# Optimization experiments

Hardware: AMD Instinct MI355X
Metric: run time of the kernel (lower is better)

Reference implementation:

```python
import jax, jax.numpy as jnp
import numpy as np

NQUBIT = 24
CHI = 512
Q = 2
MID_SCALE = 1.0 / 32.0  # 1/sqrt(Q*CHI): keeps the sequential bond-matrix product O(1)


def _to_c(x):
    # x[..., 0] = real part, x[..., 1] = imag part -> complex64
    return jax.lax.complex(x[..., 0], x[..., 1])


def setup_inputs() -> dict:
    key = jax.random.key(0)
    k1, k2, k3 = jax.random.split(key, 3)
    t_first = jax.random.normal(k1, (1, Q, CHI, 2), dtype=jnp.float32)
    t_mid = jax.random.normal(k2, (NQUBIT - 2, CHI, Q, CHI, 2), dtype=jnp.float32) * MID_SCALE
    t_last = jax.random.normal(k3, (CHI, Q, 1, 2), dtype=jnp.float32)
    return {"t_first": t_first, "t_mid": t_mid, "t_last": t_last}


def _sweep(t_first, t_mid, t_last):
    # Faithful translation of center_orthogonalization(c=-1):
    # left-to-right orthogonalize_left2right over sites 0..nqubit-2, dc=-1 (no
    # truncation), normalize=False. Each step: SVD of (Dl*q, Dr) reshape,
    # keep u as the new site tensor, absorb r = diag(s) @ vh into the next site
    # via einsum 'ab,bcd->acd'. Returns the center (last) tensor.
    tensors = [_to_c(t_first)] + [_to_c(t_mid[i]) for i in range(NQUBIT - 2)] + [_to_c(t_last)]
    for i in range(NQUBIT - 1):  # loop over sites (structural, shapes differ per site)
        t = tensors[i]
        Dl, q, Dr = t.shape
        u, s, vh = jnp.linalg.svd(t.reshape(Dl * q, Dr), full_matrices=False)
        tensors[i] = u.reshape(Dl, q, -1)            # left-orthogonal site tensor
        r = s.astype(vh.dtype)[:, None] * vh          # diag(s) @ vh, shape (k, Dr)
        tensors[i + 1] = jnp.einsum('ab,bcd->acd', r, tensors[i + 1])
    c = tensors[-1]  # center tensor, shape (CHI, Q, 1) complex64
    return jnp.stack([jnp.real(c), jnp.imag(c)], axis=-1)  # (CHI, Q, 1, 2) float32


def reference(t_first, t_mid, t_last):
    return _sweep(t_first, t_mid, t_last)
```

## Files before the change

kernel.cpp:

```cpp
#include <hip/hip_runtime.h>
#include <math.h>


#define LDV 513
typedef float2 cplx;

__device__ __forceinline__ cplx cmul(cplx a, cplx b){ return make_float2(a.x*b.x - a.y*b.y, a.x*b.y + a.y*b.x); }
__device__ __forceinline__ cplx cmulc(cplx a, cplx b){  return make_float2(a.x*b.x + a.y*b.y, a.x*b.y - a.y*b.x); }
__device__ __forceinline__ cplx cadd(cplx a, cplx b){ return make_float2(a.x+b.x, a.y+b.y); }
__device__ __forceinline__ cplx csub(cplx a, cplx b){ return make_float2(a.x-b.x, a.y-b.y); }
__device__ __forceinline__ cplx conjc(cplx a){ return make_float2(a.x, -a.y); }

#define EPS_S 5.9604645e-8f
#define UNFL_S 1.17549435e-38f
#define UW 512
#define UBLK 128

__device__ cplx g_A[1024*512];
__device__ cplx g_B[512*512];
__device__ cplx g_VTc[512*512];
__device__ cplx g_R[512*512];
__device__ cplx g_tauf[520];
__device__ cplx g_taup[520];
__device__ float g_d[520], g_e[520];
__device__ float g_VTr[LDV*LDV];
__device__ float g_VT2[LDV*LDV];
__device__ float g_W[LDV*LDV];
__device__ float g_z[520], g_zz[520], g_zorig[520], g_dtmp[520], g_ztmp[520], g_dsig[520];
__device__ double g_root[520];
__device__ int g_idxq[520], g_idx[520], g_idxp[520], g_rowmap[520];
__device__ int g_inode[80], g_ndiml[80], g_ndimr[80];
__device__ float g_sig[520];
__device__ int g_K, g_nlvl_, g_nd_;
__device__ float g_tol_, g_z1_;
__device__ double g_rho_;
__device__ float g_scq[520];
__device__ float g_betaq[520];
__device__ float g_rn[520];
__device__ float g_partC[UW];
__device__ float g_partR[UW];

__device__ __forceinline__ float wred(float v){
  for (int off=32;off;off>>=1) v+=__shfl_down(v,off);
  return v;
}
__device__ __forceinline__ float reduce512(const float* arr){
  __shared__ float sr[256];
  sr[threadIdx.x]=arr[threadIdx.x]+arr[threadIdx.x+256];
  __syncthreads();
  for (int s=128;s>0;s>>=1){
    if (threadIdx.x<s) sr[threadIdx.x]+=sr[threadIdx.x+s];
    __syncthreads();
  }
  float v=sr[0];
  __syncthreads();
  return v;
}

struct RfgOut { float beta; cplx tau; cplx scal; int skip; };
__device__ RfgOut clarfg_head(cplx alpha, float xn2){
  RfgOut o;
  if (xn2==0.f && alpha.y==0.f){
    o.beta=alpha.x; o.tau=make_float2(0.f,0.f); o.scal=make_float2(0.f,0.f); o.skip=1;
  } else {
    float anorm=sqrtf(alpha.x*alpha.x+alpha.y*alpha.y+xn2);
    float beta=(alpha.x>=0.f)?-anorm:anorm;
    o.beta=beta;
    o.tau=make_float2((beta-alpha.x)/beta,-alpha.y/beta);
    cplx dd=make_float2(alpha.x-beta,alpha.y);
    float dn=dd.x*dd.x+dd.y*dd.y;
    o.scal=make_float2(dd.x/dn,-dd.y/dn);
    o.skip=0;
  }
  return o;
}

__device__ float slapy2(float x, float y){
  float xa=fabsf(x), ya=fabsf(y);
  float w=fmaxf(xa,ya), z=fminf(xa,ya);
  if (z==0.f) return w;
  float q=z/w; return w*sqrtf(1.f+q*q);
}

__device__ void slartg(float f, float g, float* cs, float* sn, float* r){
  if (g==0.f){ *cs=1.f; *sn=0.f; *r=f; }
  else if (f==0.f){ *cs=0.f; *sn=(g>0.f)?1.f:-1.f; *r=fabsf(g); }
  else {
    float f1=fabsf(f);
    float d=sqrtf(f*f+g*g);
    *cs = f1/d;
    *r = (f>0.f)? d : -d;
    *sn = g / *r;
  }
}

__device__ void slas2(float f, float g, float h, float* ssmin, float* ssmax){
  float fa=fabsf(f), ga=fabsf(g), ha=fabsf(h);
  float fhmn=fminf(fa,ha), fhmx=fmaxf(fa,ha);
  if (fhmn==0.f){
    *ssmin=0.f;
    if (fhmx==0.f) *ssmax=ga;
    else { float mx=fmaxf(fhmx,ga), mn=fminf(fhmx,ga); float q=mn/mx; *ssmax=mx*sqrtf(1.f+q*q); }
  } else {
    if (ga < fhmx){
      float as=1.f+fhmn/fhmx, at=(fhmx-fhmn)/fhmx;
      float au=ga/fhmx; au=au*au;
      float c=2.f/(sqrtf(as*as+au)+sqrtf(at*at+au));
      *ssmin=fhmn*c; *ssmax=fhmx/c;
    } else {
      float au=fhmx/ga;
      if (au==0.f){ *ssmin=(fhmn*fhmx)/ga; *ssmax=ga; }
      else {
        float as=1.f+fhmn/fhmx, at=(fhmx-fhmn)/fhmx;
        float c=1.f/(sqrtf(1.f+(as*au)*(as*au))+sqrtf(1.f+(at*au)*(at*au)));
        *ssmin=(fhmn*c)*au; *ssmin=*ssmin+*ssmin;
        *ssmax=ga/(c+c);
      }
    }
  }
}

__device__ void slasv2(float f, float g, float h, float* ssmin, float* ssmax,
                       float* snr, float* csr, float* snl, float* csl){
  float ft=f, fa=fabsf(f), ht=h, ha=fabsf(h);
  int pmax=1;
  bool swap_=(ha>fa);
  if (swap_){ pmax=3; float t=ft; ft=ht; ht=t; t=fa; fa=ha; ha=t; }
  float gt=g, ga=fabsf(g);
  float clt=0.f, crt=0.f, slt=0.f, srt=0.f;
  if (ga==0.f){ *ssmin=ha; *ssmax=fa; clt=1.f; crt=1.f; slt=0.f; srt=0.f; }
  else {
    bool gasmal=true;
    if (ga>fa){
      pmax=2;
      if ((fa/ga) < EPS_S){
        gasmal=false;
        *ssmax=ga;
        if (ha>1.f) *ssmin=fa/(ga/ha); else *ssmin=(fa/ga)*ha;
        clt=1.f; slt=ht/gt; srt=1.f; crt=ft/gt;
      }
    }
    if (gasmal){
      float d=fa-ha;
      float l=(d==fa)?1.f:(d/fa);
      float mm=gt/ft;
      float t=2.f-l;
      float mm2=mm*mm, tt=t*t;
      float s=sqrtf(tt+mm2);
      float r=(l==0.f)?fabsf(mm):sqrtf(l*l+mm2);
      float a=0.5f*(s+r);
      *ssmin=ha/a; *ssmax=fa*a;
      if (mm2==0.f){
        if (l==0.f) t=copysignf(2.f,ft)*copysignf(1.f,gt);
        else t=gt/copysignf(d,ft)+mm/t;
      } else {
        t=(mm/(s+t)+mm/(r+l))*(1.f+a);
      }
      float l2=sqrtf(t*t+4.f);
      crt=2.f/l2; srt=t/l2;
      clt=(crt+srt*mm)/a;
      slt=(ht/ft)*srt/a;
    }
  }
  if (swap_){ *csl=srt; *snl=crt; *csr=slt; *snr=clt; }
  else      { *csl=clt; *snl=slt; *csr=crt; *snr=srt; }
  float tsign=0.f;
  if (pmax==1) tsign=copysignf(1.f,*csr)*copysignf(1.f,*csl)*copysignf(1.f,f);
  if (pmax==2) tsign=copysignf(1.f,*snr)*copysignf(1.f,*csl)*copysignf(1.f,g);
  if (pmax==3) tsign=copysignf(1.f,*snr)*copysignf(1.f,*snl)*copysignf(1.f,h);
  *ssmax=copysignf(*ssmax,tsign);
  *ssmin=copysignf(*ssmin,tsign*copysignf(1.f,f)*copysignf(1.f,h));
}

__device__ void slasr_f(int mrows, int ncols, const float* c1, const float* s1, float* a, int lda){
  for (int j=1;j<=mrows-1;++j){
    float ct=c1[j], st=s1[j];
    if (ct!=1.f || st!=0.f){
      float* rj=&a[(j-1)*lda]; float* rj1=&a[j*lda];
      for (int i=0;i<ncols;++i){
        float tmp=rj1[i];
        rj1[i]=ct*tmp-st*rj[i];
        rj[i]=st*tmp+ct*rj[i];
      }
    }
  }
}
__device__ void slasr_b(int mrows, int ncols, const float* c1, const float* s1, float* a, int lda){
  for (int j=mrows-1;j>=1;--j){
    float ct=c1[j], st=s1[j];
    if (ct!=1.f || st!=0.f){
      float* rj=&a[(j-1)*lda]; float* rj1=&a[j*lda];
      for (int i=0;i<ncols;++i){
        float tmp=rj1[i];
        rj1[i]=ct*tmp-st*rj[i];
        rj[i]=st*tmp+ct*rj[i];
      }
    }
  }
}

__device__ void sbdsqr_u(int n, int ncvt, float* d, float* e, float* vt, int ldvt){
  const int MAXITR=6;
  if (n==0) return;
  if (n>1){
    int nm1=n-1, nm12=nm1+nm1, nm13=nm12+nm1;
    float wk[112];
    float tolmul=10.f;
    float tol=tolmul*EPS_S;
    float smax=0.f;
    for (int i=1;i<=n;i++) smax=fmaxf(smax,fabsf(d[i]));
    for (int i=1;i<=n-1;i++) smax=fmaxf(smax,fabsf(e[i]));
    float sminl=0.f, thresh;
    {
      float sminoa=fabsf(d[1]);
      if (sminoa!=0.f){
        float mu=sminoa;
        for (int i=2;i<=n;i++){
          mu=fabsf(d[i])*(mu/(mu+fabsf(e[i-1])));
          sminoa=fminf(sminoa,mu);
          if (sminoa==0.f) break;
        }
      }
      sminoa=sminoa/sqrtf((float)n);
      thresh=fmaxf(tol*sminoa,(float)(MAXITR*n*n)*UNFL_S);
    }
    int M=n, iter=0, maxit=MAXITR*n*n;
    int oldll=-1, oldm=-1, idir=0;
    while (1){
      if (M<=1) break;
      if (iter>maxit) break;
      int ll=0; bool split=false;
      smax=fabsf(d[M]);
      for (int lll=1;lll<=M-1;++lll){
        ll=M-lll;
        float abss=fabsf(d[ll]), abse=fabsf(e[ll]);
        if (abse<=thresh){ split=true; break; }
        smax=fmaxf(smax,fmaxf(abss,abse));
      }
      if (!split) ll=0;
      else {
        e[ll]=0.f;
        if (ll==M-1){ M=M-1; continue; }
      }
      ll=ll+1;
      if (ll==M-1){
        float sigmn,sigmx,sinr,cosr,sinl,cosl;
        slasv2(d[M-1],e[M-1],d[M],&sigmn,&sigmx,&sinr,&cosr,&sinl,&cosl);
        d[M-1]=sigmx; e[M-1]=0.f; d[M]=sigmn;
        if (ncvt>0){
          float* x=&vt[(M-2)*ldvt]; float* y=&vt[(M-1)*ldvt];
          for (int c=0;c<ncvt;c++){ float xv=x[c],yv=y[c]; x[c]=cosr*xv+sinr*yv; y[c]=cosr*yv-sinr*xv; }
        }
        M-=2; continue;
      }
      if (ll>oldm || M<oldll) idir=(fabsf(d[ll])>=fabsf(d[M]))?1:2;
      bool conv=false;
      if (idir==1){
        if (fabsf(e[M-1])<=fabsf(tol)*fabsf(d[M])){ e[M-1]=0.f; conv=true; }
        else {
          float mu=fabsf(d[ll]); sminl=mu;
          for (int lll=ll;lll<=M-1;++lll){
            if (fabsf(e[lll])<=tol*mu){ e[lll]=0.f; conv=true; break; }
            mu=fabsf(d[lll+1])*(mu/(mu+fabsf(e[lll])));
            sminl=fminf(sminl,mu);
          }
        }
      } else {
        if (fabsf(e[ll])<=fabsf(tol)*fabsf(d[ll])){ e[ll]=0.f; conv=true; }
        else {
          float mu=fabsf(d[M]); sminl=mu;
          for (int lll=M-1;lll>=ll;--lll){
            if (fabsf(e[lll])<=tol*mu){ e[lll]=0.f; conv=true; break; }
            mu=fabsf(d[lll])*(mu/(mu+fabsf(e[lll])));
            sminl=fminf(sminl,mu);
          }
        }
      }
      if (conv) continue;
      oldll=ll; oldm=M;
      float shift=0.f, rr;
      if ((float)n*tol*(sminl/smax)<=fmaxf(EPS_S,0.01f*tol)) shift=0.f;
      else {
        float sll;
        if (idir==1){ sll=fabsf(d[ll]); slas2(d[M-1],e[M-1],d[M],&shift,&rr); }
        else        { sll=fabsf(d[M]);  slas2(d[ll],e[ll],d[ll+1],&shift,&rr); }
        if (sll>0.f){ float q=shift/sll; if (q*q<EPS_S) shift=0.f; }
      }
      iter += M-ll;
      if (shift==0.f){
        if (idir==1){
          float cs=1.f, oldcs=1.f, sn=0.f, oldsn=0.f;
          for (int i=ll;i<=M-1;++i){
            float c2,r1;
            slartg(d[i]*cs,e[i],&c2,&sn,&r1); cs=c2;
            if (i>ll) e[i-1]=oldsn*r1;
            float oc2;
            slartg(oldcs*r1,d[i+1]*sn,&oc2,&oldsn,&d[i]); oldcs=oc2;
            wk[i-ll+1]=cs; wk[i-ll+1+nm1]=sn;
          }
          float h=d[M]*cs; d[M]=h*oldcs; e[M-1]=h*oldsn;
          if (ncvt>0) slasr_f(M-ll+1,ncvt,wk,wk+nm1,&vt[(ll-1)*ldvt],ldvt);
          if (fabsf(e[M-1])<=thresh) e[M-1]=0.f;
        } else {
          float cs=1.f, oldcs=1.f, sn=0.f, oldsn=0.f;
          for (int i=M;i>=ll+1;--i){
            float c2,r1;
            slartg(d[i]*cs,e[i-1],&c2,&sn,&r1); cs=c2;
            if (i<M) e[i]=oldsn*r1;
            float oc2;
            slartg(oldcs*r1,d[i-1]*sn,&oc2,&oldsn,&d[i]); oldcs=oc2;
            wk[i-ll]=cs; wk[i-ll+nm1]=-sn;
            wk[i-ll+nm12]=oldcs; wk[i-ll+nm13]=-oldsn;
          }
          float h=d[ll]*cs; d[ll]=h*oldcs; e[ll]=h*oldsn;
          if (ncvt>0) slasr_b(M-ll+1,ncvt,wk+nm12,wk+nm13,&vt[(ll-1)*ldvt],ldvt);
          if (fabsf(e[ll])<=thresh) e[ll]=0.f;
        }
      } else {
        if (idir==1){
          float f=(fabsf(d[ll])-shift)*(copysignf(1.f,d[ll])+shift/d[ll]);
          float g=e[ll], cosr,sinr,cosl,sinl,r1;
          for (int i=ll;i<=M-1;++i){
            slartg(f,g,&cosr,&sinr,&r1);
            if (i>ll) e[i-1]=r1;
            f=cosr*d[i]+sinr*e[i];
            e[i]=cosr*e[i]-sinr*d[i];
            g=sinr*d[i+1];
            d[i+1]=cosr*d[i+1];
            slartg(f,g,&cosl,&sinl,&r1);
            d[i]=r1;
            f=cosl*e[i]+sinl*d[i+1];
            d[i+1]=cosl*d[i+1]-sinl*e[i];
            if (i<M-1){ g=sinl*e[i+1]; e[i+1]=cosl*e[i+1]; }
            wk[i-ll+1]=cosr; wk[i-ll+1+nm1]=sinr;
            wk[i-ll+1+nm12]=cosl; wk[i-ll+1+nm13]=sinl;
          }
          e[M-1]=f;
          if (ncvt>0) slasr_f(M-ll+1,ncvt,wk,wk+nm1,&vt[(ll-1)*ldvt],ldvt);
          if (fabsf(e[M-1])<=thresh) e[M-1]=0.f;
        } else {
          float f=(fabsf(d[M])-shift)*(copysignf(1.f,d[M])+shift/d[M]);
          float g=e[M-1], cosr,sinr,cosl,sinl,r1;
          for (int i=M;i>=ll+1;--i){
            slartg(f,g,&cosr,&sinr,&r1);
            if (i<M) e[i]=r1;
            f=cosr*d[i]+sinr*e[i-1];
            e[i-1]=cosr*e[i-1]-sinr*d[i];
            g=sinr*d[i-1];
            d[i-1]=cosr*d[i-1];
            slartg(f,g,&cosl,&sinl,&r1);
            d[i]=r1;
            f=cosl*e[i-1]+sinl*d[i-1];
            d[i-1]=cosl*d[i-1]-sinl*e[i-1];
            if (i>ll+1){ g=sinl*e[i-2]; e[i-2]=cosl*e[i-2]; }
            wk[i-ll]=cosr; wk[i-ll+nm1]=-sinr;
            wk[i-ll+nm12]=cosl; wk[i-ll+nm13]=-sinl;
          }
          e[ll]=f;
          if (fabsf(e[ll])<=thresh) e[ll]=0.f;
          if (ncvt>0) slasr_b(M-ll+1,ncvt,wk+nm12,wk+nm13,&vt[(ll-1)*ldvt],ldvt);
        }
      }
    }
  }
  for (int i=1;i<=n;i++){
    if (d[i]<0.f){
      d[i]=-d[i];
      if (ncvt>0){ float* row=&vt[(i-1)*ldvt]; for (int c=0;c<ncvt;c++) row[c]=-row[c]; }
    }
  }
  for (int i=1;i<=n-1;i++){
    int isub=1; float smin2=d[1];
    for (int j=2;j<=n+1-i;j++){ if (d[j]<=smin2){ isub=j; smin2=d[j]; } }
    if (isub!=n+1-i){
      d[isub]=d[n+1-i]; d[n+1-i]=smin2;
      if (ncvt>0){
        float* a=&vt[(isub-1)*ldvt]; float* b=&vt[(n-i)*ldvt];
        for (int c=0;c<ncvt;c++){ float t=a[c]; a[c]=b[c]; b[c]=t; }
      }
    }
  }
}

__device__ void slasdq_u(int sqre, int n, int ncvt, float* d, float* e, float* vt, int ldvt){
  if (n==0) return;
  float cwk[33], swk[33];
  int np1=n+1;
  if (sqre==1){
    for (int i=1;i<=n-1;i++){
      float cs,sn,r; slartg(d[i],e[i],&cs,&sn,&r);
      d[i]=r; e[i]=sn*d[i+1]; d[i+1]=cs*d[i+1];
      cwk[i]=cs; swk[i]=sn;
    }
    { float cs,sn,r; slartg(d[n],e[n],&cs,&sn,&r);
      d[n]=r; e[n]=0.f; cwk[n]=cs; swk[n]=sn; }
    if (ncvt>0) slasr_f(np1,ncvt,cwk,swk,vt,ldvt);
    for (int i=1;i<=n-1;i++){
      float cs,sn,r; slartg(d[i],e[i],&cs,&sn,&r);
      d[i]=r; e[i]=sn*d[i+1]; d[i+1]=cs*d[i+1];
    }
  }
  sbdsqr_u(n,ncvt,d,e,vt,ldvt);
  for (int i=1;i<=n;i++){
    int isub=i; float smin2=d[i];
    for (int j=i+1;j<=n;j++){ if (d[j]<smin2){ isub=j; smin2=d[j]; } }
    if (isub!=i){
      d[isub]=d[i]; d[i]=smin2;
      if (ncvt>0){
        float* a=&vt[(isub-1)*ldvt]; float* b=&vt[(i-1)*ldvt];
        for (int c=0;c<ncvt;c++){ float t=a[c]; a[c]=b[c]; b[c]=t; }
      }
    }
  }
}

__device__ void slamrg(int n1, int n2, const float* a, int s1, int s2, int* idx){
  int n1sv=n1, n2sv=n2, i=1;
  int ind1=(s1>0)?1:n1;
  int ind2=(s2>0)?(1+n1):(n1+n2);
  while (n1sv>0 && n2sv>0){
    if (a[ind1]<=a[ind2]){ idx[i++]=ind1; ind1+=s1; n1sv--; }
    else { idx[i++]=ind2; ind2+=s2; n2sv--; }
  }
  if (n1sv==0){ for(;n2sv>0;n2sv--){ idx[i++]=ind2; ind2+=s2; } }
  else { for(;n1sv>0;n1sv--){ idx[i++]=ind1; ind1+=s1; } }
}

__device__ void slasdt(int n, int* lvl, int* nd, int* inode, int* ndiml, int* ndimr, int msub){
  int maxn=(n>1)?n:1;
  float temp=logf((float)maxn/(float)(msub+1))/logf(2.f);
  *lvl=(int)temp+1;
  int i=n/2;
  inode[1]=i+1; ndiml[1]=i; ndimr[1]=n-i-1;
  int il=0, ir=1, llst=1;
  for (int nl=1;nl<=*lvl-1;++nl){
    for (int j=0;j<=llst-1;++j){
      il+=2; ir+=2;
      int nc=llst+j;
      ndiml[il]=ndiml[nc]/2;
      ndimr[il]=ndiml[nc]-ndiml[il]-1;
      inode[il]=inode[nc]-ndimr[il]-1;
      ndiml[ir]=ndimr[nc]/2;
      ndimr[ir]=ndimr[nc]-ndiml[ir]-1;
      inode[ir]=inode[nc]+ndiml[ir]+1;
    }
    llst*=2;
  }
  *nd=llst*2-1;
}

__device__ void merge_node(int nl, int nr, int sqre, float* d, int* idxq,
                           float alpha, float beta, float* VT, int ld)
{
  const int tid=threadIdx.x, nth=blockDim.x;
  const int n=nl+nr+1, m=n+sqre, nlp1=nl+1, nlp2=nl+2;
  if (tid==0){
    float* z=g_z;
    float z1=alpha*VT[(nlp1-1)*ld+(nlp1-1)];
    z[1]=z1; g_z1_=z1;
    for (int i=nl;i>=1;--i){
      z[i+1]=alpha*VT[(i-1)*ld+(nlp1-1)];
      d[i+1]=d[i];
      idxq[i+1]=idxq[i]+1;
    }
    for (int i=nlp2;i<=m;++i) z[i]=beta*VT[(i-1)*ld+(nlp2-1)];
    d[1]=0.f;
    for (int i=nlp2;i<=n;++i) idxq[i]+=nlp1;
    for (int i=2;i<=n;++i){ g_dtmp[i]=d[idxq[i]]; g_ztmp[i]=z[idxq[i]]; }
    slamrg(nl,nr,g_dtmp+1,1,1,g_idx+1);
    for (int i=2;i<=n;++i){
      int idxi=1+g_idx[i];
      d[i]=g_dtmp[idxi];
      z[i]=g_ztmp[idxi];
    }
    float tol=fmaxf(fabsf(alpha),fabsf(beta));
    tol=8.f*EPS_S*fmaxf(fabsf(d[n]),tol);
    g_tol_=tol;
    int K=1, K2=n+1, jprev=0, j;
    for (j=2;j<=n;++j){
      if (fabsf(z[j])<=tol){
        K2--; g_idxp[K2]=j;
        if (j==n){ jprev=0; break; }
      } else { jprev=j; break; }
    }
    if (jprev>0){
      j=jprev;
      for (;;){
        j++;
        if (j>n) break;
        if (fabsf(z[j])<=tol){ K2--; g_idxp[K2]=j; }
        else {
          if (fabsf(d[j]-d[jprev])<=tol){
            float s_=z[jprev], c_=z[j];
            float tau_=slapy2(c_,s_);
            c_/=tau_; s_=-s_/tau_;
            z[j]=tau_; z[jprev]=0.f;
            int idxjp=idxq[g_idx[jprev]+1];
            int idxj =idxq[g_idx[j]+1];
            if (idxjp<=nlp1) idxjp--;
            if (idxj <=nlp1) idxj--;
            float* xr=&VT[(idxjp-1)*ld];
            float* yr=&VT[(idxj-1)*ld];
            for (int cc=0;cc<m;++cc){
              float xv=xr[cc], yv=yr[cc];
              xr[cc]=c_*xv+s_*yv;
              yr[cc]=c_*yv-s_*xv;
            }
            K2--; g_idxp[K2]=jprev;
            jprev=j;
          } else {
            K++; g_zz[K]=z[jprev]; g_idxp[K]=jprev;
            jprev=j;
          }
        }
      }
      K++; g_zz[K]=z[jprev]; g_idxp[K]=jprev;
    }
    g_K=K;
    for (int jj=2;jj<=n;++jj){
      g_dsig[jj]=d[g_idxp[jj]];
      int rm=idxq[g_idx[g_idxp[jj]]+1];
      if (rm<=nlp1) rm--;
      g_rowmap[jj]=rm;
    }
  }
  __syncthreads();
  int K=g_K;
  for (int t=tid;t<(n-1)*m;t+=nth){
    int jj=2+t/m, cc=t%m;
    g_VT2[(jj-1)*LDV+cc]=VT[(g_rowmap[jj]-1)*ld+cc];
  }
  __syncthreads();
  if (tid==0){
    float tol=g_tol_;
    g_dsig[1]=0.f;
    float hlftol=tol*0.5f;
    if (fabsf(g_dsig[2])<=hlftol) g_dsig[2]=hlftol;
    float z1=g_z1_;
    float c_=1.f, s_=0.f;
    if (m>n){
      float t1=slapy2(z1,g_z[m]);
      if (t1<=tol){ c_=1.f; s_=0.f; g_z[1]=tol; }
      else { g_z[1]=t1; c_=z1/t1; s_=g_z[m]/t1; }
    } else {
      if (fabsf(z1)<=tol) g_z[1]=tol; else g_z[1]=z1;
    }
    for (int jj=2;jj<=K;++jj) g_z[jj]=g_zz[jj];
    if (m>n){
      for (int i=1;i<=nlp1;++i){
        float v=VT[(nlp1-1)*ld+(i-1)];
        VT[(m-1)*ld+(i-1)]=-s_*v;
        g_VT2[(i-1)]=c_*v;
      }
      for (int i=nlp2;i<=m;++i){
        float v=VT[(m-1)*ld+(i-1)];
        g_VT2[(i-1)]=s_*v;
        VT[(m-1)*ld+(i-1)]=c_*v;
      }
    } else {
      for (int i=1;i<=m;++i) g_VT2[(i-1)]=VT[(nlp1-1)*ld+(i-1)];
    }
    for (int jj=K+1;jj<=n;++jj) d[jj]=g_dsig[jj];
    double rho=0.0;
    for (int jj=1;jj<=K;++jj){ double zz2=(double)g_z[jj]; rho+=zz2*zz2; g_zorig[jj]=g_z[jj]; }
    g_rho_=rho;
  }
  __syncthreads();
  for (int t=tid;t<(n-K)*m;t+=nth){
    int jj=K+1+t/m, cc=t%m;
    VT[(jj-1)*ld+cc]=g_VT2[(jj-1)*LDV+cc];
  }
  __syncthreads();
  if (K==1){
    if (tid==0){
      d[1]=fabsf(g_z[1]);
      for (int cc=0;cc<m;++cc) VT[cc]=g_VT2[cc];
      slamrg(1,n-1,d,1,-1,idxq);
    }
    __syncthreads();
    return;
  }
  {
    double rho=g_rho_;
    for (int i=1+tid;i<=K;i+=nth){
      double di=(double)g_dsig[i];
      double lo=di*di, hi;
      if (i<K){ double dn=(double)g_dsig[i+1]; hi=dn*dn; }
      else { double dn=(double)g_dsig[K]; hi=dn*dn+rho; }
      for (int it=0;it<110;++it){
        double mid=0.5*(lo+hi);
        double f=1.0;
        for (int j=1;j<=K;++j){
          double dj=(double)g_dsig[j];
          double zj=(double)g_z[j];
          f+=zj*zj/(dj*dj-mid);
        }
        if (f>=0.0) hi=mid; else lo=mid;
      }
      g_root[i]=0.5*(lo+hi);
      d[i]=(float)sqrt(g_root[i]);
    }
  }
  __syncthreads();
  for (int i=1+tid;i<=K;i+=nth){
    double di=(double)g_dsig[i], di2=di*di;
    double p=di2-g_root[K];
    for (int j=1;j<=i-1;++j){
      double dj=(double)g_dsig[j];
      p*=(di2-g_root[j])/((di-dj)*(di+dj));
    }
    for (int j=i;j<=K-1;++j){
      double dj1=(double)g_dsig[j+1];
      p*=(di2-g_root[j])/((di-dj1)*(di+dj1));
    }
    g_ztmp[i]=copysignf((float)sqrt(fabs(p)),g_zorig[i]);
  }
  __syncthreads();
  for (int i=1+tid;i<=K;i+=nth) g_z[i]=g_ztmp[i];
  __syncthreads();
  for (int i=1+tid;i<=K;i+=nth){
    double xi=g_root[i];
    double nrm=0.0;
    for (int j=1;j<=K;++j){
      double dj=(double)g_dsig[j];
      double w=(double)g_z[j]/(dj*dj-xi);
      g_W[(i-1)*LDV+(j-1)]=(float)w;
      nrm+=w*w;
    }
    float inv=(float)(1.0/sqrt(nrm));
    for (int j=1;j<=K;++j) g_W[(i-1)*LDV+(j-1)]*=inv;
  }
  __syncthreads();
  for (int t=tid;t<K*m;t+=nth){
    int i=1+t/m, cc=t%m;
    float acc=0.f;
    for (int j=1;j<=K;++j)
      acc=fmaf(g_W[(i-1)*LDV+(j-1)],g_VT2[(j-1)*LDV+cc],acc);
    VT[(i-1)*ld+cc]=acc;
  }
  __syncthreads();
  if (tid==0) slamrg(K,n-K,d,1,-1,idxq);
  __syncthreads();
}

__global__ __launch_bounds__(1024) void k_sbdsdc(int n){
  const int tid=threadIdx.x, lane=tid&63, wv=tid>>6;
  for (int t=tid;t<n*n;t+=1024)
    g_VTr[(t/n)*LDV+(t%n)]=((t/n)==(t%n))?1.f:0.f;
  __syncthreads();
  if (n<=25){
    if (tid==0){
      slasdq_u(0,n,n,g_d,g_e,g_VTr,LDV);
      for (int j=1;j<=n;++j) g_idxq[j]=j;
    }
    __syncthreads();
  } else {
    if (tid==0){
      int lvl,nd;
      slasdt(n,&lvl,&nd,g_inode,g_ndiml,g_ndimr,25);
      g_nlvl_=lvl; g_nd_=nd;
    }
    __syncthreads();
    int nd=g_nd_, nlvl=g_nlvl_;
    int ndb1=(nd+1)/2;
    int ntask=(nd-ndb1+1)*2;
    for (int task=wv;task<ntask;task+=16){
      if (lane==0){
        int node=ndb1+(task>>1);
        int ic=g_inode[node], nl=g_ndiml[node], nr=g_ndimr[node];
        if ((task&1)==0){
          int nlf=ic-nl;
          slasdq_u(1,nl,nl+1,g_d+(nlf-1),g_e+(nlf-1),&g_VTr[(nlf-1)*LDV+(nlf-1)],LDV);
          for (int j2=1;j2<=nl;++j2) g_idxq[nlf-1+j2]=j2;
        } else {
          int nrf=ic+1;
          int sq=(node==nd)?0:1;
          slasdq_u(sq,nr,nr+sq,g_d+(nrf-1),g_e+(nrf-1),&g_VTr[(nrf-1)*LDV+(nrf-1)],LDV);
          for (int j2=1;j2<=nr;++j2) g_idxq[nrf-1+j2]=j2;
        }
      }
    }
    __syncthreads();
    for (int lvl=nlvl;lvl>=1;--lvl){
      int lf=(lvl==1)?1:(1<<(lvl-1));
      int llast=(lvl==1)?1:(2*lf-1);
      for (int node=lf;node<=llast;++node){
        int ic=g_inode[node], nl=g_ndiml[node], nr=g_ndimr[node];
        int nlf=ic-nl;
        int sq=(node==llast)?0:1;
        float alpha=g_d[ic], beta=g_e[ic];
        merge_node(nl,nr,sq,g_d+(nlf-1),g_idxq+(nlf-1),alpha,beta,
                   &g_VTr[(nlf-1)*LDV+(nlf-1)],LDV);
      }
    }
  }
  __syncthreads();
  for (int t=tid;t<n*512;t+=1024){
    int i=t/512, c=t%512;
    int o=g_idxq[n-i];
    float v=(c<n)?g_VTr[(o-1)*LDV+c]:0.f;
    g_VTc[i*512+c]=make_float2(v,0.f);
    if (c==0) g_sig[i]=g_d[o];
  }
}

__global__ void k_m0(const float* __restrict__ tf){
  int i=blockIdx.x*blockDim.x+threadIdx.x;
  if (i<1024) g_A[i]=make_float2(tf[2*i],tf[2*i+1]);
}

__global__ __launch_bounds__(1024) void k_lq(int m){
  const int n=512;
  const int tid=threadIdx.x, lane=tid&63, wv=tid>>6;
  __shared__ float s_part[16];
  __shared__ cplx s_tau, s_scal;
  __shared__ float s_beta; __shared__ int s_skip;
  for (int i=1;i<=m;++i){
    for (int c=i+tid;c<=n;c+=1024) g_A[(i-1)*512+(c-1)].y=-g_A[(i-1)*512+(c-1)].y;
    __syncthreads();
    float sq=0.f;
    for (int c=i+1+tid;c<=n;c+=1024){
      cplx a=g_A[(i-1)*512+(c-1)];
      sq=fmaf(a.x,a.x,fmaf(a.y,a.y,sq));
    }
    sq=wred(sq);
    if (lane==0) s_part[wv]=sq;
    __syncthreads();
    if (tid==0){
      float xn2=0.f; for (int w=0;w<16;w++) xn2+=s_part[w];
      RfgOut o=clarfg_head(g_A[(i-1)*512+(i-1)],xn2);
      s_beta=o.beta; s_tau=o.tau; s_scal=o.scal; s_skip=o.skip;
      g_tauf[i]=o.tau;
    }
    __syncthreads();
    if (!s_skip){
      for (int c=i+1+tid;c<=n;c+=1024)
        g_A[(i-1)*512+(c-1)]=cmul(g_A[(i-1)*512+(c-1)],s_scal);
    }
    __syncthreads();
    if (!s_skip){
      cplx tau=s_tau;
      for (int r=i+1+wv;r<=m;r+=16){
        cplx acc=make_float2(0.f,0.f);
        for (int c=i+lane;c<=n;c+=64){
          cplx u=(c==i)?make_float2(1.f,0.f):g_A[(i-1)*512+(c-1)];
          acc=cadd(acc,cmul(g_A[(r-1)*512+(c-1)],u));
        }
        acc.x=wred(acc.x); acc.y=wred(acc.y);
        acc.x=__shfl(acc.x,0); acc.y=__shfl(acc.y,0);
        cplx tw=cmul(tau,acc);
        for (int c=i+lane;c<=n;c+=64){
          cplx u=(c==i)?make_float2(1.f,0.f):g_A[(i-1)*512+(c-1)];
          g_A[(r-1)*512+(c-1)]=csub(g_A[(r-1)*512+(c-1)],cmul(tw,conjc(u)));
        }
      }
    }
    __syncthreads();
    if (tid==0) g_A[(i-1)*512+(i-1)]=make_float2(s_beta,0.f);
    __syncthreads();
  }
}

__global__ void k_copyL(int m){
  int t=blockIdx.x*blockDim.x+threadIdx.x;
  if (t>=m*m) return;
  int r=t/m, c=t%m;
  g_B[r*512+c]=(c<=r)?g_A[r*512+c]:make_float2(0.f,0.f);
}
__global__ void k_copyM(){
  int t=blockIdx.x*blockDim.x+threadIdx.x;
  if (t<512*512) g_B[t]=g_A[t];
}
__global__ void k_copyR_b(){
  int t=blockIdx.x*blockDim.x+threadIdx.x;
  if (t>=512*512) return;
  int r=t/512, c=t%512;
  g_B[t]=(c>r)?g_A[t]:((c==r)?make_float2(g_betaq[r+1],0.f):make_float2(0.f,0.f));
}

__global__ __launch_bounds__(1024) void k_bd(int n){
  const int tid=threadIdx.x, lane=tid&63, wv=tid>>6;
  __shared__ float s_part[16];
  __shared__ cplx s_tau, s_scal;
  __shared__ float s_beta; __shared__ int s_skip;
  for (int i=1;i<=n;++i){
    float sq=0.f;
    for (int r=i+1+tid;r<=n;r+=1024){
      cplx a=g_B[(r-1)*512+(i-1)];
      sq=fmaf(a.x,a.x,fmaf(a.y,a.y,sq));
    }
    sq=wred(sq);
    if (lane==0) s_part[wv]=sq;
    __syncthreads();
    if (tid==0){
      float xn2=0.f; for (int w=0;w<16;w++) xn2+=s_part[w];
      RfgOut o=clarfg_head(g_B[(i-1)*512+(i-1)],xn2);
      s_beta=o.beta; s_tau=o.tau; s_scal=o.scal; s_skip=o.skip;
      g_d[i]=o.beta;
    }
    __syncthreads();
    if (!s_skip){
      for (int r=i+1+tid;r<=n;r+=1024)
        g_B[(r-1)*512+(i-1)]=cmul(g_B[(r-1)*512+(i-1)],s_scal);
    }
    __syncthreads();
    if (!s_skip){
      cplx tauc=conjc(s_tau);
      for (int c=i+1+wv;c<=n;c+=16){
        cplx acc=make_float2(0.f,0.f);
        for (int r=i+lane;r<=n;r+=64){
          cplx v=(r==i)?make_float2(1.f,0.f):g_B[(r-1)*512+(i-1)];
          acc=cadd(acc,cmulc(v,g_B[(r-1)*512+(c-1)]));
        }
        acc.x=wred(acc.x); acc.y=wred(acc.y);
        acc.x=__shfl(acc.x,0); acc.y=__shfl(acc.y,0);
        cplx tw=cmul(tauc,acc);
        for (int r=i+lane;r<=n;r+=64){
          cplx v=(r==i)?make_float2(1.f,0.f):g_B[(r-1)*512+(i-1)];
          g_B[(r-1)*512+(c-1)]=csub(g_B[(r-1)*512+(c-1)],cmul(tw,v));
        }
      }
    }
    __syncthreads();
    if (tid==0) g_B[(i-1)*512+(i-1)]=make_float2(s_beta,0.f);
    __syncthreads();
    if (i<n){
      for (int c=i+1+tid;c<=n;c+=1024) g_B[(i-1)*512+(c-1)].y=-g_B[(i-1)*512+(c-1)].y;
      __syncthreads();
      float sq2=0.f;
      for (int c=i+2+tid;c<=n;c+=1024){
        cplx a=g_B[(i-1)*512+(c-1)];
        sq2=fmaf(a.x,a.x,fmaf(a.y,a.y,sq2));
      }
      sq2=wred(sq2);
      if (lane==0) s_part[wv]=sq2;
      __syncthreads();
      if (tid==0){
        float xn2=0.f; for (int w=0;w<16;w++) xn2+=s_part[w];
        RfgOut o=clarfg_head(g_B[(i-1)*512+(i)],xn2);
        s_beta=o.beta; s_tau=o.tau; s_scal=o.scal; s_skip=o.skip;
        g_e[i]=o.beta; g_taup[i]=o.tau;
      }
      __syncthreads();
      if (!s_skip){
        for (int c=i+2+tid;c<=n;c+=1024)
          g_B[(i-1)*512+(c-1)]=cmul(g_B[(i-1)*512+(c-1)],s_scal);
      }
      __syncthreads();
      if (!s_skip){
        cplx tau=s_tau;
        for (int r=i+1+wv;r<=n;r+=16){
          cplx acc=make_float2(0.f,0.f);
          for (int c=i+1+lane;c<=n;c+=64){
            cplx v=(c==i+1)?make_float2(1.f,0.f):g_B[(i-1)*512+(c-1)];
            acc=cadd(acc,cmul(g_B[(r-1)*512+(c-1)],v));
          }
          acc.x=wred(acc.x); acc.y=wred(acc.y);
          acc.x=__shfl(acc.x,0); acc.y=__shfl(acc.y,0);
          cplx tw=cmul(tau,acc);
          for (int c=i+1+lane;c<=n;c+=64){
            cplx v=(c==i+1)?make_float2(1.f,0.f):g_B[(i-1)*512+(c-1)];
            g_B[(r-1)*512+(c-1)]=csub(g_B[(r-1)*512+(c-1)],cmul(tw,conjc(v)));
          }
        }
      }
      __syncthreads();
      for (int c=i+2+tid;c<=n;c+=1024) g_B[(i-1)*512+(c-1)].y=-g_B[(i-1)*512+(c-1)].y;
      if (tid==0) g_B[(i-1)*512+(i)]=make_float2(s_beta,0.f);
      __syncthreads();
    }
  }
}

__global__ __launch_bounds__(1024) void k_applyPH(int n){
  const int tid=threadIdx.x, lane=tid&63, wv=tid>>6;
  for (int i=n-1;i>=1;--i){
    cplx tau=g_taup[i];
    if (tau.x==0.f && tau.y==0.f) continue;
    cplx tauc=conjc(tau);
    for (int r=1+wv;r<=n;r+=16){
      cplx acc=make_float2(0.f,0.f);
      for (int c=i+1+lane;c<=n;c+=64){
        cplx v=(c==i+1)?make_float2(1.f,0.f):conjc(g_B[(i-1)*512+(c-1)]);
        acc=cadd(acc,cmul(g_VTc[(r-1)*512+(c-1)],v));
      }
      acc.x=wred(acc.x); acc.y=wred(acc.y);
      acc.x=__shfl(acc.x,0); acc.y=__shfl(acc.y,0);
      cplx tw=cmul(tauc,acc);
      for (int c=i+1+lane;c<=n;c+=64){
        cplx vb=(c==i+1)?make_float2(1.f,0.f):g_B[(i-1)*512+(c-1)];
        g_VTc[(r-1)*512+(c-1)]=csub(g_VTc[(r-1)*512+(c-1)],cmul(tw,vb));
      }
    }
    __syncthreads();
  }
}

__global__ __launch_bounds__(1024) void k_applyQlq(int m){
  const int tid=threadIdx.x, lane=tid&63, wv=tid>>6;
  for (int i=m;i>=1;--i){
    cplx tau=g_tauf[i];
    if (tau.x==0.f && tau.y==0.f) continue;
    cplx tauc=conjc(tau);
    for (int r=1+wv;r<=m;r+=16){
      cplx acc=make_float2(0.f,0.f);
      for (int c=i+lane;c<=512;c+=64){
        cplx u=(c==i)?make_float2(1.f,0.f):g_A[(i-1)*512+(c-1)];
        acc=cadd(acc,cmul(g_VTc[(r-1)*512+(c-1)],u));
      }
      acc.x=wred(acc.x); acc.y=wred(acc.y);
      acc.x=__shfl(acc.x,0); acc.y=__shfl(acc.y,0);
      cplx tw=cmul(tauc,acc);
      for (int c=i+lane;c<=512;c+=64){
        cplx u=(c==i)?make_float2(1.f,0.f):g_A[(i-1)*512+(c-1)];
        g_VTc[(r-1)*512+(c-1)]=csub(g_VTc[(r-1)*512+(c-1)],cmul(tw,conjc(u)));
      }
    }
    __syncthreads();
  }
}


__global__ __launch_bounds__(256) void u_qr_pro(){
  __shared__ float sr[256];
  int t=threadIdx.x;
  float sq=0.f;
  for (int r=2+t;r<=1024;r+=256){ cplx a=g_A[(r-1)*512]; sq=fmaf(a.x,a.x,fmaf(a.y,a.y,sq)); }
  sr[t]=sq; __syncthreads();
  for (int s=128;s>0;s>>=1){ if (t<s) sr[t]+=sr[t+s]; __syncthreads(); }
  if (t==0) g_scq[1]=sr[0];
}

__global__ __launch_bounds__(256) void u_qr(int j){
  const int m=1024, n=512;
  int gtid=blockIdx.x*256+threadIdx.x;
  int lane=gtid&63, gw=gtid>>6;
  float xn2=g_scq[j];
  cplx alpha=g_A[(j-1)*512+(j-1)];
  RfgOut o=clarfg_head(alpha,xn2);
  if (gtid==0) g_betaq[j]=o.beta;
  cplx tauc=conjc(o.tau);
  float nsq=0.f;
  for (int c=j+1+gw;c<=n;c+=UW){
    cplx acc=make_float2(0.f,0.f);
    for (int r=j+lane;r<=m;r+=64){
      cplx v=(r==j)?make_float2(1.f,0.f):cmul(g_A[(r-1)*512+(j-1)],o.scal);
      acc=cadd(acc,cmulc(v,g_A[(r-1)*512+(c-1)]));
    }
    acc.x=wred(acc.x); acc.y=wred(acc.y);
    acc.x=__shfl(acc.x,0); acc.y=__shfl(acc.y,0);
    cplx tw=cmul(tauc,acc);
    for (int r=j+lane;r<=m;r+=64){
      cplx v=(r==j)?make_float2(1.f,0.f):cmul(g_A[(r-1)*512+(j-1)],o.scal);
      cplx nv=csub(g_A[(r-1)*512+(c-1)],cmul(tw,v));
      g_A[(r-1)*512+(c-1)]=nv;
      if (c==j+1 && r>=j+2) nsq=fmaf(nv.x,nv.x,fmaf(nv.y,nv.y,nsq));
    }
  }
  if (gw==0){
    nsq=wred(nsq);
    if (lane==0) g_scq[j+1]=nsq;
  }
}

__global__ __launch_bounds__(512) void u_bd_pro(){
  int t=threadIdx.x;
  float sq=0.f;
  for (int r=2+t;r<=512;r+=512){ cplx a=g_B[(r-1)*512]; sq=fmaf(a.x,a.x,fmaf(a.y,a.y,sq)); }
  g_partR[t]=sq;
}

__global__ __launch_bounds__(256) void u_bd_col(int i){
  const int n=512;
  float xn2c=reduce512(g_partR);
  int gtid=blockIdx.x*256+threadIdx.x;
  int lane=gtid&63, gw=gtid>>6;
  cplx alpha=g_B[(i-1)*512+(i-1)];
  RfgOut oc=clarfg_head(alpha,xn2c);
  if (gtid==0) g_d[i]=oc.beta;
  cplx tauc=conjc(oc.tau);
  float nsqA=0.f;
  for (int c=i+1+gw;c<=n;c+=UW){
    cplx acc=make_float2(0.f,0.f);
    for (int r=i+lane;r<=n;r+=64){
      cplx v=(r==i)?make_float2(1.f,0.f):cmul(g_B[(r-1)*512+(i-1)],oc.scal);
      acc=cadd(acc,cmulc(v,g_B[(r-1)*512+(c-1)]));
    }
    acc.x=wred(acc.x); acc.y=wred(acc.y);
    acc.x=__shfl(acc.x,0); acc.y=__shfl(acc.y,0);
    cplx tw=cmul(tauc,acc);
    for (int r=i+lane;r<=n;r+=64){
      cplx v=(r==i)?make_float2(1.f,0.f):cmul(g_B[(r-1)*512+(i-1)],oc.scal);
      cplx nv=csub(g_B[(r-1)*512+(c-1)],cmul(tw,v));
      g_B[(r-1)*512+(c-1)]=nv;
      if (r==i && c>=i+2) nsqA=fmaf(nv.x,nv.x,fmaf(nv.y,nv.y,nsqA));
    }
  }
  if (lane==0) g_partC[gw]=nsqA;
}

__global__ __launch_bounds__(256) void u_bd_row(int i){
  const int n=512;
  float xn2r=reduce512(g_partC);
  int gtid=blockIdx.x*256+threadIdx.x;
  int lane=gtid&63, gw=gtid>>6;
  cplx alphar=conjc(g_B[(i-1)*512+(i)]);
  RfgOut orr=clarfg_head(alphar,xn2r);
  if (gtid==0){ g_e[i]=orr.beta; g_taup[i]=orr.tau; g_rn[i]=xn2r; }
  float nsqB=0.f;
  for (int r=i+1+gw;r<=n;r+=UW){
    cplx acc=make_float2(0.f,0.f);
    for (int c=i+1+lane;c<=n;c+=64){
      cplx v=(c==i+1)?make_float2(1.f,0.f):cmul(conjc(g_B[(i-1)*512+(c-1)]),orr.scal);
      acc=cadd(acc,cmul(g_B[(r-1)*512+(c-1)],v));
    }
    acc.x=wred(acc.x); acc.y=wred(acc.y);
    acc.x=__shfl(acc.x,0); acc.y=__shfl(acc.y,0);
    cplx tw=cmul(orr.tau,acc);
    for (int c=i+1+lane;c<=n;c+=64){
      cplx v=(c==i+1)?make_float2(1.f,0.f):cmul(conjc(g_B[(i-1)*512+(c-1)]),orr.scal);
      cplx nv=csub(g_B[(r-1)*512+(c-1)],cmul(tw,conjc(v)));
      g_B[(r-1)*512+(c-1)]=nv;
      if (c==i+1 && r>=i+2) nsqB=fmaf(nv.x,nv.x,fmaf(nv.y,nv.y,nsqB));
    }
  }
  if (lane==0) g_partR[gw]=nsqB;
}

__global__ __launch_bounds__(256) void u_ph(){
  const int n=512;
  int b=blockIdx.x;
  int wv=threadIdx.x>>6, lane=threadIdx.x&63;
  int r=b*4+wv+1;
  for (int i=n-1;i>=1;--i){
    cplx alphar=conjc(g_B[(i-1)*512+(i)]);
    RfgOut o=clarfg_head(alphar,g_rn[i]);
    if (o.skip) continue;
    cplx tauc=conjc(o.tau);
    cplx acc=make_float2(0.f,0.f);
    for (int c=i+1+lane;c<=n;c+=64){
      cplx v=(c==i+1)?make_float2(1.f,0.f):cmul(conjc(g_B[(i-1)*512+(c-1)]),o.scal);
      acc=cadd(acc,cmul(g_VTc[(r-1)*512+(c-1)],v));
    }
    acc.x=wred(acc.x); acc.y=wred(acc.y);
    acc.x=__shfl(acc.x,0); acc.y=__shfl(acc.y,0);
    cplx tw=cmul(tauc,acc);
    for (int c=i+1+lane;c<=n;c+=64){
      cplx v=(c==i+1)?make_float2(1.f,0.f):cmul(conjc(g_B[(i-1)*512+(c-1)]),o.scal);
      g_VTc[(r-1)*512+(c-1)]=csub(g_VTc[(r-1)*512+(c-1)],cmul(tw,conjc(v)));
    }
  }
}

__global__ void k_formR(int kk){
  int t=blockIdx.x*blockDim.x+threadIdx.x;
  if (t>=kk*512) return;
  float s=g_sig[t/512];
  cplx v=g_VTc[t];
  g_R[t]=make_float2(s*v.x,s*v.y);
}

__global__ void k_next(const float* __restrict__ tmid, int site){
  int row=blockIdx.x;
  int a=row>>1, s=row&1;
  int b=blockIdx.y*blockDim.x+threadIdx.x;
  const float* base=tmid+(size_t)site*512*2*512*2;
  cplx acc=make_float2(0.f,0.f);
  for (int c=0;c<512;++c){
    cplx r=g_R[a*512+c];
    size_t off=((((size_t)c)*2+s)*512+b)*2;
    cplx x=make_float2(base[off],base[off+1]);
    acc=cadd(acc,cmul(r,x));
  }
  g_A[row*512+b]=acc;
}

__global__ void k_final(const float* __restrict__ tlast, float* __restrict__ out){
  int a=blockIdx.x*blockDim.x+threadIdx.x;
  if (a>=512) return;
  for (int s=0;s<2;++s){
    cplx acc=make_float2(0.f,0.f);
    for (int c=0;c<512;++c){
      cplx r=g_R[a*512+c];
      cplx x=make_float2(tlast[(c*2+s)*2],tlast[(c*2+s)*2+1]);
      acc=cadd(acc,cmul(r,x));
    }
    out[a*4+s*2+0]=acc.x;
    out[a*4+s*2+1]=acc.y;
  }
}

extern "C" void kernel_launch(void* const* d_in, const int* in_sizes, int n_in,
                              void* d_out, int out_size, void* d_ws, size_t ws_size,
                              hipStream_t stream) {
  const float* t_first=(const float*)d_in[0];
  const float* t_mid  =(const float*)d_in[1];
  const float* t_last =(const float*)d_in[2];
  float* out=(float*)d_out;
  (void)in_sizes; (void)n_in; (void)d_ws; (void)ws_size; (void)out_size;

  k_m0<<<dim3(4),256,0,stream>>>(t_first);

  int rows=2;
  for (int site=0;site<23;++site){
    int mm=rows;
    int nb=(mm<512)?mm:512;
    if (mm<512){
      k_lq<<<1,1024,0,stream>>>(mm);
      k_copyL<<<dim3((mm*mm+255)/256),256,0,stream>>>(mm);
      k_bd<<<1,1024,0,stream>>>(mm);
      k_sbdsdc<<<1,1024,0,stream>>>(mm);
      k_applyPH<<<1,1024,0,stream>>>(mm);
      k_applyQlq<<<1,1024,0,stream>>>(mm);
    } else {
      if (mm==512){
        k_copyM<<<dim3((512*512+255)/256),256,0,stream>>>();
      } else {
        u_qr_pro<<<1,256,0,stream>>>();
        for (int j=1;j<=512;++j) u_qr<<<UBLK,256,0,stream>>>(j);
        k_copyR_b<<<dim3((512*512+255)/256),256,0,stream>>>();
      }
      u_bd_pro<<<1,512,0,stream>>>();
      for (int i=1;i<=512;++i){
        u_bd_col<<<UBLK,256,0,stream>>>(i);
        if (i<512) u_bd_row<<<UBLK,256,0,stream>>>(i);
      }
      k_sbdsdc<<<1,1024,0,stream>>>(512);
      u_ph<<<UBLK,256,0,stream>>>();
    }
    k_formR<<<dim3((nb*512+255)/256),256,0,stream>>>(nb);
    if (site<22){
      k_next<<<dim3(2*nb,2),256,0,stream>>>(t_mid,site);
      rows=2*nb;
    } else {
      k_final<<<dim3(2),256,0,stream>>>(t_last,out);
    }
  }
}
```

Before: 1.080 s.

## Replace per-step kernel launches with persistent kernels using a software grid barrier

The per-column Householder QR launches (512 kernels) and the bidiagonalization launches (about 1023 kernels) are each merged into one persistent kernel with 128 blocks, which synchronize through an atomic-counter grid barrier. This removes launch overhead and inter-kernel gaps on the roughly 1500 serialized small steps per large site. The barrier relies on all 128 blocks being co-resident without a cooperative launch. On timeout it sets a fail flag and silently stops synchronizing, which could corrupt results.

Result: slower. 1.567 s, median of 2 (+45.1%).

```diff
diff --git a/kernel.cpp b/kernel.cpp
--- a/kernel.cpp
+++ b/kernel.cpp
@@ -39,6 +39,32 @@
 __device__ float g_rn[520];
 __device__ float g_partC[UW];
 __device__ float g_partR[UW];
+__device__ unsigned g_barc = 0;
+__device__ unsigned g_barg = 0;
+__device__ int g_barfail = 0;
+
+__device__ __forceinline__ void gbar(){
+  __syncthreads();
+  if (threadIdx.x==0){
+    if (!g_barfail){
+      __threadfence();
+      unsigned gen=__hip_atomic_load(&g_barg,__ATOMIC_RELAXED,__HIP_MEMORY_SCOPE_AGENT);
+      unsigned prev=__hip_atomic_fetch_add(&g_barc,1u,__ATOMIC_ACQ_REL,__HIP_MEMORY_SCOPE_AGENT);
+      if (prev+1u==(unsigned)gridDim.x){
+        __hip_atomic_store(&g_barc,0u,__ATOMIC_RELAXED,__HIP_MEMORY_SCOPE_AGENT);
+        __hip_atomic_store(&g_barg,gen+1u,__ATOMIC_RELEASE,__HIP_MEMORY_SCOPE_AGENT);
+      } else {
+        long k=0;
+        while (__hip_atomic_load(&g_barg,__ATOMIC_ACQUIRE,__HIP_MEMORY_SCOPE_AGENT)==gen){
+          __builtin_amdgcn_s_sleep(2);
+          if (++k>(1L<<24)){ g_barfail=1; break; }
+        }
+      }
+      __threadfence();
+    }
+  }
+  __syncthreads();
+}
 
 __device__ __forceinline__ float wred(float v){
   for (int off=32;off;off>>=1) v+=__shfl_down(v,off);
@@ -921,110 +947,116 @@
 }
 
 
-__global__ __launch_bounds__(256) void u_qr_pro(){
-  __shared__ float sr[256];
-  int t=threadIdx.x;
-  float sq=0.f;
-  for (int r=2+t;r<=1024;r+=256){ cplx a=g_A[(r-1)*512]; sq=fmaf(a.x,a.x,fmaf(a.y,a.y,sq)); }
-  sr[t]=sq; __syncthreads();
-  for (int s=128;s>0;s>>=1){ if (t<s) sr[t]+=sr[t+s]; __syncthreads(); }
-  if (t==0) g_scq[1]=sr[0];
-}
-
-__global__ __launch_bounds__(256) void u_qr(int j){
+__global__ __launch_bounds__(256) void pk_qr(){
   const int m=1024, n=512;
-  int gtid=blockIdx.x*256+threadIdx.x;
-  int lane=gtid&63, gw=gtid>>6;
-  float xn2=g_scq[j];
-  cplx alpha=g_A[(j-1)*512+(j-1)];
-  RfgOut o=clarfg_head(alpha,xn2);
-  if (gtid==0) g_betaq[j]=o.beta;
-  cplx tauc=conjc(o.tau);
-  float nsq=0.f;
-  for (int c=j+1+gw;c<=n;c+=UW){
-    cplx acc=make_float2(0.f,0.f);
-    for (int r=j+lane;r<=m;r+=64){
-      cplx v=(r==j)?make_float2(1.f,0.f):cmul(g_A[(r-1)*512+(j-1)],o.scal);
-      acc=cadd(acc,cmulc(v,g_A[(r-1)*512+(c-1)]));
-    }
-    acc.x=wred(acc.x); acc.y=wred(acc.y);
-    acc.x=__shfl(acc.x,0); acc.y=__shfl(acc.y,0);
-    cplx tw=cmul(tauc,acc);
-    for (int r=j+lane;r<=m;r+=64){
-      cplx v=(r==j)?make_float2(1.f,0.f):cmul(g_A[(r-1)*512+(j-1)],o.scal);
-      cplx nv=csub(g_A[(r-1)*512+(c-1)],cmul(tw,v));
-      g_A[(r-1)*512+(c-1)]=nv;
-      if (c==j+1 && r>=j+2) nsq=fmaf(nv.x,nv.x,fmaf(nv.y,nv.y,nsq));
-    }
-  }
-  if (gw==0){
-    nsq=wred(nsq);
-    if (lane==0) g_scq[j+1]=nsq;
-  }
-}
-
-__global__ __launch_bounds__(512) void u_bd_pro(){
-  int t=threadIdx.x;
-  float sq=0.f;
-  for (int r=2+t;r<=512;r+=512){ cplx a=g_B[(r-1)*512]; sq=fmaf(a.x,a.x,fmaf(a.y,a.y,sq)); }
-  g_partR[t]=sq;
-}
-
-__global__ __launch_bounds__(256) void u_bd_col(int i){
+  const int gtid=blockIdx.x*256+threadIdx.x;
+  const int lane=gtid&63, gw=gtid>>6;
+  {
+    __shared__ float sr[256];
+    int t=threadIdx.x;
+    float sq=0.f;
+    for (int r=2+t;r<=1024;r+=256){ cplx a=g_A[(r-1)*512]; sq=fmaf(a.x,a.x,fmaf(a.y,a.y,sq)); }
+    sr[t]=sq; __syncthreads();
+    for (int s=128;s>0;s>>=1){ if (t<s) sr[t]+=sr[t+s]; __syncthreads(); }
+    if (gtid==0) g_scq[1]=sr[0];
+  }
+  gbar();
+  for (int j=1;j<=n;++j){
+    float xn2=g_scq[j];
+    cplx alpha=g_A[(j-1)*512+(j-1)];
+    RfgOut o=clarfg_head(alpha,xn2);
+    if (gtid==0) g_betaq[j]=o.beta;
+    cplx tauc=conjc(o.tau);
+    float nsq=0.f;
+    for (int c=j+1+gw;c<=n;c+=UW){
+      cplx acc=make_float2(0.f,0.f);
+      for (int r=j+lane;r<=m;r+=64){
+        cplx v=(r==j)?make_float2(1.f,0.f):cmul(g_A[(r-1)*512+(j-1)],o.scal);
+        acc=cadd(acc,cmulc(v,g_A[(r-1)*512+(c-1)]));
+      }
+      acc.x=wred(acc.x); acc.y=wred(acc.y);
+      acc.x=__shfl(acc.x,0); acc.y=__shfl(acc.y,0);
+      cplx tw=cmul(tauc,acc);
+      for (int r=j+lane;r<=m;r+=64){
+        cplx v=(r==j)?make_float2(1.f,0.f):cmul(g_A[(r-1)*512+(j-1)],o.scal);
+        cplx nv=csub(g_A[(r-1)*512+(c-1)],cmul(tw,v));
+        g_A[(r-1)*512+(c-1)]=nv;
+        if (c==j+1 && r>=j+2) nsq=fmaf(nv.x,nv.x,fmaf(nv.y,nv.y,nsq));
+      }
+    }
+    if (gw==0){
+      nsq=wred(nsq);
+      if (lane==0) g_scq[j+1]=nsq;
+    }
+    gbar();
+  }
+}
+
+__global__ __launch_bounds__(256) void pk_bd(){
   const int n=512;
-  float xn2c=reduce512(g_partR);
-  int gtid=blockIdx.x*256+threadIdx.x;
-  int lane=gtid&63, gw=gtid>>6;
-  cplx alpha=g_B[(i-1)*512+(i-1)];
-  RfgOut oc=clarfg_head(alpha,xn2c);
-  if (gtid==0) g_d[i]=oc.beta;
-  cplx tauc=conjc(oc.tau);
-  float nsqA=0.f;
-  for (int c=i+1+gw;c<=n;c+=UW){
-    cplx acc=make_float2(0.f,0.f);
-    for (int r=i+lane;r<=n;r+=64){
-      cplx v=(r==i)?make_float2(1.f,0.f):cmul(g_B[(r-1)*512+(i-1)],oc.scal);
-      acc=cadd(acc,cmulc(v,g_B[(r-1)*512+(c-1)]));
-    }
-    acc.x=wred(acc.x); acc.y=wred(acc.y);
-    acc.x=__shfl(acc.x,0); acc.y=__shfl(acc.y,0);
-    cplx tw=cmul(tauc,acc);
-    for (int r=i+lane;r<=n;r+=64){
-      cplx v=(r==i)?make_float2(1.f,0.f):cmul(g_B[(r-1)*512+(i-1)],oc.scal);
-      cplx nv=csub(g_B[(r-1)*512+(c-1)],cmul(tw,v));
-      g_B[(r-1)*512+(c-1)]=nv;
-      if (r==i && c>=i+2) nsqA=fmaf(nv.x,nv.x,fmaf(nv.y,nv.y,nsqA));
-    }
-  }
-  if (lane==0) g_partC[gw]=nsqA;
-}
-
-__global__ __launch_bounds__(256) void u_bd_row(int i){
-  const int n=512;
-  float xn2r=reduce512(g_partC);
-  int gtid=blockIdx.x*256+threadIdx.x;
-  int lane=gtid&63, gw=gtid>>6;
-  cplx alphar=conjc(g_B[(i-1)*512+(i)]);
-  RfgOut orr=clarfg_head(alphar,xn2r);
-  if (gtid==0){ g_e[i]=orr.beta; g_taup[i]=orr.tau; g_rn[i]=xn2r; }
-  float nsqB=0.f;
-  for (int r=i+1+gw;r<=n;r+=UW){
-    cplx acc=make_float2(0.f,0.f);
-    for (int c=i+1+lane;c<=n;c+=64){
-      cplx v=(c==i+1)?make_float2(1.f,0.f):cmul(conjc(g_B[(i-1)*512+(c-1)]),orr.scal);
-      acc=cadd(acc,cmul(g_B[(r-1)*512+(c-1)],v));
-    }
-    acc.x=wred(acc.x); acc.y=wred(acc.y);
-    acc.x=__shfl(acc.x,0); acc.y=__shfl(acc.y,0);
-    cplx tw=cmul(orr.tau,acc);
-    for (int c=i+1+lane;c<=n;c+=64){
-      cplx v=(c==i+1)?make_float2(1.f,0.f):cmul(conjc(g_B[(i-1)*512+(c-1)]),orr.scal);
-      cplx nv=csub(g_B[(r-1)*512+(c-1)],cmul(tw,conjc(v)));
-      g_B[(r-1)*512+(c-1)]=nv;
-      if (c==i+1 && r>=i+2) nsqB=fmaf(nv.x,nv.x,fmaf(nv.y,nv.y,nsqB));
-    }
-  }
-  if (lane==0) g_partR[gw]=nsqB;
+  const int gtid=blockIdx.x*256+threadIdx.x;
+  const int lane=gtid&63, gw=gtid>>6;
+  if (blockIdx.x<2){
+    int t=gtid;
+    float sq=0.f;
+    for (int r=2+t;r<=512;r+=512){ cplx a=g_B[(r-1)*512]; sq=fmaf(a.x,a.x,fmaf(a.y,a.y,sq)); }
+    g_partR[t]=sq;
+  }
+  gbar();
+  for (int i=1;i<=n;++i){
+    {
+      float xn2c=reduce512(g_partR);
+      cplx alpha=g_B[(i-1)*512+(i-1)];
+      RfgOut oc=clarfg_head(alpha,xn2c);
+      if (gtid==0) g_d[i]=oc.beta;
+      cplx tauc=conjc(oc.tau);
+      float nsqA=0.f;
+      for (int c=i+1+gw;c<=n;c+=UW){
+        cplx acc=make_float2(0.f,0.f);
+        for (int r=i+lane;r<=n;r+=64){
+          cplx v=(r==i)?make_float2(1.f,0.f):cmul(g_B[(r-1)*512+(i-1)],oc.scal);
+          acc=cadd(acc,cmulc(v,g_B[(r-1)*512+(c-1)]));
+        }
+        acc.x=wred(acc.x); acc.y=wred(acc.y);
+        acc.x=__shfl(acc.x,0); acc.y=__shfl(acc.y,0);
+        cplx tw=cmul(tauc,acc);
+        for (int r=i+lane;r<=n;r+=64){
+          cplx v=(r==i)?make_float2(1.f,0.f):cmul(g_B[(r-1)*512+(i-1)],oc.scal);
+          cplx nv=csub(g_B[(r-1)*512+(c-1)],cmul(tw,v));
+          g_B[(r-1)*512+(c-1)]=nv;
+          if (r==i && c>=i+2) nsqA=fmaf(nv.x,nv.x,fmaf(nv.y,nv.y,nsqA));
+        }
+      }
+      if (lane==0) g_partC[gw]=nsqA;
+    }
+    gbar();
+    if (i==n) break;
+    {
+      float xn2r=reduce512(g_partC);
+      cplx alphar=conjc(g_B[(i-1)*512+(i)]);
+      RfgOut orr=clarfg_head(alphar,xn2r);
+      if (gtid==0){ g_e[i]=orr.beta; g_taup[i]=orr.tau; g_rn[i]=xn2r; }
+      float nsqB=0.f;
+      for (int r=i+1+gw;r<=n;r+=UW){
+        cplx acc=make_float2(0.f,0.f);
+        for (int c=i+1+lane;c<=n;c+=64){
+          cplx v=(c==i+1)?make_float2(1.f,0.f):cmul(conjc(g_B[(i-1)*512+(c-1)]),orr.scal);
+          acc=cadd(acc,cmul(g_B[(r-1)*512+(c-1)],v));
+        }
+        acc.x=wred(acc.x); acc.y=wred(acc.y);
+        acc.x=__shfl(acc.x,0); acc.y=__shfl(acc.y,0);
+        cplx tw=cmul(orr.tau,acc);
+        for (int c=i+1+lane;c<=n;c+=64){
+          cplx v=(c==i+1)?make_float2(1.f,0.f):cmul(conjc(g_B[(i-1)*512+(c-1)]),orr.scal);
+          cplx nv=csub(g_B[(r-1)*512+(c-1)],cmul(tw,conjc(v)));
+          g_B[(r-1)*512+(c-1)]=nv;
+          if (c==i+1 && r>=i+2) nsqB=fmaf(nv.x,nv.x,fmaf(nv.y,nv.y,nsqB));
+        }
+      }
+      if (lane==0) g_partR[gw]=nsqB;
+    }
+    gbar();
+  }
 }
 
 __global__ __launch_bounds__(256) void u_ph(){
@@ -1116,15 +1148,10 @@
       if (mm==512){
         k_copyM<<<dim3((512*512+255)/256),256,0,stream>>>();
       } else {
-        u_qr_pro<<<1,256,0,stream>>>();
-        for (int j=1;j<=512;++j) u_qr<<<UBLK,256,0,stream>>>(j);
+        pk_qr<<<UBLK,256,0,stream>>>();
         k_copyR_b<<<dim3((512*512+255)/256),256,0,stream>>>();
       }
-      u_bd_pro<<<1,512,0,stream>>>();
-      for (int i=1;i<=512;++i){
-        u_bd_col<<<UBLK,256,0,stream>>>(i);
-        if (i<512) u_bd_row<<<UBLK,256,0,stream>>>(i);
-      }
+      pk_bd<<<UBLK,256,0,stream>>>();
       k_sbdsdc<<<1,1024,0,stream>>>(512);
       u_ph<<<UBLK,256,0,stream>>>();
     }
```
